# Kernel tuning notes

Hardware: AMD Instinct MI355X
Metric: run time of the kernel (lower is better)

The kernel has to match this reference:

```python
import jax, jax.numpy as jnp
import numpy as np

DIM = 1024; NH = 16; HD = DIM // NH          # head_dim = 64
E = 8; K = 2; TEMP = 1.0; HID = 1024         # routed experts / top-k / moe_inter_dim
SHID = HID * 1                               # shared expert hidden (n_shared_experts=1)
EPS = 1e-6


def _rms(x, w):
    return x * jax.lax.rsqrt(jnp.mean(x * x, axis=-1, keepdims=True) + EPS) * w


def setup_inputs() -> dict:
    key = jax.random.key(0)
    ks = jax.random.split(key, 16)
    B, S = 2, 2048
    x = jax.random.normal(ks[0], (B, S, DIM), jnp.float32)
    # RoPE table: (S, HD//2, 2) with [..., 0]=cos, [..., 1]=sin  (theta=10000)
    inv = 1.0 / (10000.0 ** (jnp.arange(0, HD, 2, dtype=jnp.float32) / HD))
    ang = jnp.arange(S, dtype=jnp.float32)[:, None] * inv[None, :]
    freqs = jnp.stack([jnp.cos(ang), jnp.sin(ang)], axis=-1)
    sc = 0.02
    W = lambda k, shape: jax.random.normal(k, shape, jnp.float32) * sc
    return dict(
        x=x, freqs=freqs,
        att_norm_w=jnp.ones((DIM,), jnp.float32),
        wq=W(ks[1], (DIM, DIM)), wk=W(ks[2], (DIM, DIM)),
        wv=W(ks[3], (DIM, DIM)), wo=W(ks[4], (DIM, DIM)),
        ffn_norm_w=jnp.ones((DIM,), jnp.float32),
        gate_w=W(ks[5], (E, DIM)),
        ew1=W(ks[6], (E, DIM, HID)), ew2=W(ks[7], (E, HID, DIM)), ew3=W(ks[8], (E, DIM, HID)),
        sw1=W(ks[9], (DIM, SHID)), sw2=W(ks[10], (SHID, DIM)), sw3=W(ks[11], (DIM, SHID)),
    )


def reference(x, freqs, att_norm_w, wq, wk, wv, wo, ffn_norm_w, gate_w,
              ew1, ew2, ew3, sw1, sw2, sw3):
    B, S, _ = x.shape
    # --- attention sub-block ---
    xn = _rms(x, att_norm_w)
    q = (xn @ wq).reshape(B, S, NH, HD)
    k = (xn @ wk).reshape(B, S, NH, HD)
    v = (xn @ wv).reshape(B, S, NH, HD)
    cos = freqs[:S, :, 0][None, :, None, :]  # (1,S,1,HD//2)
    sin = freqs[:S, :, 1][None, :, None, :]
    def rope(t):  # complex multiply on interleaved (real, imag) pairs
        t = t.reshape(B, S, NH, HD // 2, 2)
        r = t[..., 0] * cos - t[..., 1] * sin
        i = t[..., 0] * sin + t[..., 1] * cos
        return jnp.stack([r, i], axis=-1).reshape(B, S, NH, HD)
    q = rope(q); k = rope(k)
    q = q.transpose(0, 2, 1, 3); k = k.transpose(0, 2, 1, 3); v = v.transpose(0, 2, 1, 3)
    scores = jnp.einsum('bhqd,bhkd->bhqk', q, k) / np.sqrt(HD).astype(np.float32)
    probs = jax.nn.softmax(scores.astype(jnp.float32), axis=-1).astype(q.dtype)
    att = jnp.einsum('bhqk,bhkd->bhqd', probs, v).transpose(0, 2, 1, 3).reshape(B, S, DIM)
    h = x + att @ wo
    # --- MoE sub-block ---
    hn = _rms(h, ffn_norm_w).reshape(-1, DIM)  # (N, DIM), N = B*S
    N = hn.shape[0]
    gate_scores = (hn @ gate_w.T) / TEMP
    gate_probs = jax.nn.softmax(gate_scores, axis=-1)
    topk_vals, topk_idx = jax.lax.top_k(gate_probs, K)
    # expert_mask[n, e] = routing weight (0 if not in top-k)
    expert_mask = jnp.zeros((N, E), hn.dtype).at[jnp.arange(N)[:, None], topk_idx].set(topk_vals)
    # dense grouped-GEMM form of the per-expert gather/compute/scatter loop;
    # tokens not routed to expert e get weight 0 => identical math
    h1 = jnp.einsum('nd,edh->enh', hn, ew1)
    h3 = jnp.einsum('nd,edh->enh', hn, ew3)
    eo = jnp.einsum('enh,ehd->end', jax.nn.silu(h1) * h3, ew2)
    y = jnp.einsum('end,ne->nd', eo, expert_mask)
    shared = (jax.nn.silu(hn @ sw1) * (hn @ sw3)) @ sw2
    return h + (y + shared).reshape(B, S, DIM)
```

## Files before the change

kernel.cpp:

```cpp
#include <hip/hip_runtime.h>

#define DIMD 1024
#define NHEAD 16
#define HDIM 64
#define SEQ 2048
#define NBATCH 2
#define NTOK 4096
#define NEXP 8
#define HIDD 1024
#define NSLOT 8192
#define MAXTILES 72
#define FA_BQ 128
#define FA_BK 64

typedef unsigned short ushort_t;
typedef __bf16 bf16x8 __attribute__((ext_vector_type(8)));
typedef float f32x4 __attribute__((ext_vector_type(4)));
typedef unsigned short ushort8v __attribute__((ext_vector_type(8)));
typedef unsigned short ushort4v __attribute__((ext_vector_type(4)));

#define GLL16(gp, lp) __builtin_amdgcn_global_load_lds( \
    (const __attribute__((address_space(1))) unsigned int*)(gp), \
    (__attribute__((address_space(3))) unsigned int*)(lp), 16, 0, 0)

__device__ inline float bf2f(ushort_t b) {
    union { unsigned int u; float f; } v; v.u = ((unsigned int)b) << 16; return v.f;
}
__device__ inline ushort_t f2bf(float f) {
    union { float f; unsigned int u; } v; v.f = f;
    unsigned int u = v.u;
    return (ushort_t)((u + 0x7FFFu + ((u >> 16) & 1u)) >> 16);
}
__device__ inline ushort_t cvt_bf16(float f) { return f2bf(f); }
__device__ inline ushort_t cvt_bf16(ushort_t u) { return u; }

template <typename Tin>
__global__ __launch_bounds__(256) void transpose_bf16(
    const Tin* __restrict__ in, ushort_t* __restrict__ out,
    int R, int C, int ld_in, int ld_out, int nb1,
    long si1, long si2, long so1, long so2)
{
    __shared__ ushort_t tile[32][33];
    int z = blockIdx.z, z1 = z % nb1, z2 = z / nb1;
    in  += (size_t)z1 * si1 + (size_t)z2 * si2;
    out += (size_t)z1 * so1 + (size_t)z2 * so2;
    int c0 = blockIdx.x * 32, r0 = blockIdx.y * 32;
    int tx = threadIdx.x & 31, ty = threadIdx.x >> 5;
#pragma unroll
    for (int i = 0; i < 4; i++) {
        int r = r0 + ty + i * 8, c = c0 + tx;
        ushort_t v = 0;
        if (r < R && c < C) v = cvt_bf16(in[(size_t)r * ld_in + c]);
        tile[ty + i * 8][tx] = v;
    }
    __syncthreads();
#pragma unroll
    for (int i = 0; i < 4; i++) {
        int cc = c0 + ty + i * 8, rr = r0 + tx;
        if (cc < C && rr < R) out[(size_t)cc * ld_out + rr] = tile[tx][ty + i * 8];
    }
}

__global__ __launch_bounds__(256) void transpose7(
    const float* __restrict__ p0, const float* __restrict__ p1, const float* __restrict__ p2,
    const float* __restrict__ p3, const float* __restrict__ p4, const float* __restrict__ p5,
    const float* __restrict__ p6, ushort_t* __restrict__ out)
{
    __shared__ ushort_t tile[32][33];
    const float* srcs[7] = {p0, p1, p2, p3, p4, p5, p6};
    const float* in = srcs[blockIdx.z];
    ushort_t* o = out + (size_t)blockIdx.z * DIMD * DIMD;
    int c0 = blockIdx.x * 32, r0 = blockIdx.y * 32;
    int tx = threadIdx.x & 31, ty = threadIdx.x >> 5;
#pragma unroll
    for (int i = 0; i < 4; i++)
        tile[ty + i * 8][tx] = f2bf(in[(size_t)(r0 + ty + i * 8) * DIMD + c0 + tx]);
    __syncthreads();
#pragma unroll
    for (int i = 0; i < 4; i++)
        o[(size_t)(c0 + ty + i * 8) * DIMD + r0 + tx] = tile[tx][ty + i * 8];
}

__global__ __launch_bounds__(256) void rmsnorm_kernel(
    const float* __restrict__ x, const float* __restrict__ w, ushort_t* __restrict__ out)
{
    size_t row = blockIdx.x;
    const float* xr = x + row * DIMD;
    int t = threadIdx.x;
    float4 xv = ((const float4*)xr)[t];
    float ss = xv.x * xv.x + xv.y * xv.y + xv.z * xv.z + xv.w * xv.w;
    for (int o = 32; o; o >>= 1) ss += __shfl_xor(ss, o, 64);
    __shared__ float red[4];
    if ((t & 63) == 0) red[t >> 6] = ss;
    __syncthreads();
    ss = red[0] + red[1] + red[2] + red[3];
    float rs = 1.0f / sqrtf(ss / (float)DIMD + 1e-6f);
    float4 wv = ((const float4*)w)[t];
    ushort4v o;
    o[0] = f2bf(xv.x * rs * wv.x); o[1] = f2bf(xv.y * rs * wv.y);
    o[2] = f2bf(xv.z * rs * wv.z); o[3] = f2bf(xv.w * rs * wv.w);
    *(ushort4v*)(out + row * DIMD + t * 4) = o;
}

template <bool OUT_BF16, bool RESID>
__global__ __launch_bounds__(256, 2) void gemm_bt(
    const ushort_t* __restrict__ A, const ushort_t* __restrict__ B,
    void* __restrict__ Cv, const float* __restrict__ Rres,
    int M, int N, int K, int lda, int ldb, int ldc,
    int nb1, long sA1, long sA2, long sB1, long sB2, long sC1, long sC2,
    float alpha)
{
    __shared__ ushort_t lsA[128][32];
    __shared__ ushort_t lsB[128][32];
    int z = blockIdx.z, z1 = z % nb1, z2 = z / nb1;
    A += (size_t)z1 * sA1 + (size_t)z2 * sA2;
    B += (size_t)z1 * sB1 + (size_t)z2 * sB2;
    size_t coff = (size_t)z1 * sC1 + (size_t)z2 * sC2;
    int tn0 = blockIdx.x * 128, tm0 = blockIdx.y * 128;
    int t = threadIdx.x;
    int wave = t >> 6, lane = t & 63;
    int wm = (wave >> 1) * 64, wn = (wave & 1) * 64;
    int lrow = lane & 15, quad = lane >> 4;
    char* lsAb = (char*)&lsA[0][0];
    char* lsBb = (char*)&lsB[0][0];
    f32x4 acc[4][4] = {};

    for (int kt = 0; kt < K; kt += 32) {
        __syncthreads();
#pragma unroll
        for (int cc = 0; cc < 2; cc++) {
            int c = t + cc * 256;
            int r = c >> 2, kc = (c & 3) * 8;
            int ar = tm0 + r; ar = (ar < M) ? ar : (M - 1);
            GLL16(A + (size_t)ar * lda + kt + kc, lsAb + (size_t)c * 16);
            int br = tn0 + r; br = (br < N) ? br : (N - 1);
            GLL16(B + (size_t)br * ldb + kt + kc, lsBb + (size_t)c * 16);
        }
        __syncthreads();
        bf16x8 afr[4], bfr[4];
#pragma unroll
        for (int i = 0; i < 4; i++) {
            afr[i] = *(const bf16x8*)(&lsA[wm + i * 16 + lrow][quad * 8]);
            bfr[i] = *(const bf16x8*)(&lsB[wn + i * 16 + lrow][quad * 8]);
        }
#pragma unroll
        for (int mi = 0; mi < 4; mi++)
#pragma unroll
            for (int ni = 0; ni < 4; ni++)
                acc[mi][ni] = __builtin_amdgcn_mfma_f32_16x16x32_bf16(
                    afr[mi], bfr[ni], acc[mi][ni], 0, 0, 0);
    }
#pragma unroll
    for (int mi = 0; mi < 4; mi++)
#pragma unroll
        for (int ni = 0; ni < 4; ni++) {
            int col = tn0 + wn + ni * 16 + lrow;
            if (col >= N) continue;
            int row0 = tm0 + wm + mi * 16 + quad * 4;
#pragma unroll
            for (int r = 0; r < 4; r++) {
                int row = row0 + r;
                if (row >= M) continue;
                size_t idx = coff + (size_t)row * ldc + col;
                float v = acc[mi][ni][r] * alpha;
                if (RESID) v += Rres[idx];
                if (OUT_BF16) ((ushort_t*)Cv)[idx] = f2bf(v);
                else          ((float*)Cv)[idx] = v;
            }
        }
}

__global__ __launch_bounds__(256, 2) void gemm_grouped(
    const ushort_t* __restrict__ A, const ushort_t* __restrict__ Bt,
    ushort_t* __restrict__ C, const int* __restrict__ perm,
    const int* __restrict__ tile_e, const int* __restrict__ tile_r0,
    const int* __restrict__ tile_r1, const int* __restrict__ ntiles, long sBe)
{
    int tt = blockIdx.y;
    if (tt >= *ntiles) return;
    int e = tile_e[tt], r0 = tile_r0[tt], r1 = tile_r1[tt];
    const ushort_t* B = Bt + (size_t)e * sBe;
    int tn0 = blockIdx.x * 128;
    __shared__ ushort_t lsA[128][32];
    __shared__ ushort_t lsB[128][32];
    int t = threadIdx.x;
    int wave = t >> 6, lane = t & 63;
    int wm = (wave >> 1) * 64, wn = (wave & 1) * 64;
    int lrow = lane & 15, quad = lane >> 4;
    char* lsAb = (char*)&lsA[0][0];
    char* lsBb = (char*)&lsB[0][0];
    f32x4 acc[4][4] = {};

    for (int kt = 0; kt < DIMD; kt += 32) {
        __syncthreads();
#pragma unroll
        for (int cc = 0; cc < 2; cc++) {
            int c = t + cc * 256;
            int r = c >> 2, kc = (c & 3) * 8;
            int sl = r0 + r; if (sl >= r1) sl = r1 - 1;
            int ar = perm ? perm[sl] : sl;
            GLL16(A + (size_t)ar * DIMD + kt + kc, lsAb + (size_t)c * 16);
            int br = tn0 + r;
            GLL16(B + (size_t)br * DIMD + kt + kc, lsBb + (size_t)c * 16);
        }
        __syncthreads();
        bf16x8 afr[4], bfr[4];
#pragma unroll
        for (int i = 0; i < 4; i++) {
            afr[i] = *(const bf16x8*)(&lsA[wm + i * 16 + lrow][quad * 8]);
            bfr[i] = *(const bf16x8*)(&lsB[wn + i * 16 + lrow][quad * 8]);
        }
#pragma unroll
        for (int mi = 0; mi < 4; mi++)
#pragma unroll
            for (int ni = 0; ni < 4; ni++)
                acc[mi][ni] = __builtin_amdgcn_mfma_f32_16x16x32_bf16(
                    afr[mi], bfr[ni], acc[mi][ni], 0, 0, 0);
    }
#pragma unroll
    for (int mi = 0; mi < 4; mi++)
#pragma unroll
        for (int ni = 0; ni < 4; ni++) {
            int col = tn0 + wn + ni * 16 + lrow;
            int l0 = wm + mi * 16 + quad * 4;
#pragma unroll
            for (int r = 0; r < 4; r++) {
                int slot = r0 + l0 + r;
                if (slot >= r1) continue;
                C[(size_t)slot * DIMD + col] = f2bf(acc[mi][ni][r]);
            }
        }
}

__global__ __launch_bounds__(256, 2) void moe_mlp1(
    const ushort_t* __restrict__ A, const ushort_t* __restrict__ B1t, const ushort_t* __restrict__ B3t,
    ushort_t* __restrict__ C, const int* __restrict__ perm,
    const int* __restrict__ tile_e, const int* __restrict__ tile_r0,
    const int* __restrict__ tile_r1, const int* __restrict__ ntiles, long sBe)
{
    int tt = blockIdx.y;
    if (tt >= *ntiles) return;
    int e = tile_e[tt], r0 = tile_r0[tt], r1 = tile_r1[tt];
    const ushort_t* B1 = B1t + (size_t)e * sBe;
    const ushort_t* B3 = B3t + (size_t)e * sBe;
    int tn0 = blockIdx.x * 128;
    __shared__ ushort_t lsA[128][32];
    __shared__ ushort_t lsB1[128][32];
    __shared__ ushort_t lsB3[128][32];
    int t = threadIdx.x;
    int wave = t >> 6, lane = t & 63;
    int wm = (wave >> 1) * 64, wn = (wave & 1) * 64;
    int lrow = lane & 15, quad = lane >> 4;
    char* lsAb  = (char*)&lsA[0][0];
    char* lsB1b = (char*)&lsB1[0][0];
    char* lsB3b = (char*)&lsB3[0][0];
    f32x4 acc1[4][4] = {};
    f32x4 acc3[4][4] = {};

    for (int kt = 0; kt < DIMD; kt += 32) {
        __syncthreads();
#pragma unroll
        for (int cc = 0; cc < 2; cc++) {
            int c = t + cc * 256;
            int r = c >> 2, kc = (c & 3) * 8;
            int sl = r0 + r; if (sl >= r1) sl = r1 - 1;
            int ar = perm ? perm[sl] : sl;
            GLL16(A + (size_t)ar * DIMD + kt + kc, lsAb + (size_t)c * 16);
            int br = tn0 + r;
            GLL16(B1 + (size_t)br * DIMD + kt + kc, lsB1b + (size_t)c * 16);
            GLL16(B3 + (size_t)br * DIMD + kt + kc, lsB3b + (size_t)c * 16);
        }
        __syncthreads();
        bf16x8 afr[4], b1fr[4], b3fr[4];
#pragma unroll
        for (int i = 0; i < 4; i++) {
            afr[i]  = *(const bf16x8*)(&lsA[wm + i * 16 + lrow][quad * 8]);
            b1fr[i] = *(const bf16x8*)(&lsB1[wn + i * 16 + lrow][quad * 8]);
            b3fr[i] = *(const bf16x8*)(&lsB3[wn + i * 16 + lrow][quad * 8]);
        }
#pragma unroll
        for (int mi = 0; mi < 4; mi++)
#pragma unroll
            for (int ni = 0; ni < 4; ni++) {
                acc1[mi][ni] = __builtin_amdgcn_mfma_f32_16x16x32_bf16(
                    afr[mi], b1fr[ni], acc1[mi][ni], 0, 0, 0);
                acc3[mi][ni] = __builtin_amdgcn_mfma_f32_16x16x32_bf16(
                    afr[mi], b3fr[ni], acc3[mi][ni], 0, 0, 0);
            }
    }
#pragma unroll
    for (int mi = 0; mi < 4; mi++)
#pragma unroll
        for (int ni = 0; ni < 4; ni++) {
            int col = tn0 + wn + ni * 16 + lrow;
            int l0 = wm + mi * 16 + quad * 4;
#pragma unroll
            for (int r = 0; r < 4; r++) {
                int slot = r0 + l0 + r;
                if (slot >= r1) continue;
                float h1 = acc1[mi][ni][r], h3 = acc3[mi][ni][r];
                float s = h1 / (1.f + __expf(-h1));
                C[(size_t)slot * DIMD + col] = f2bf(s * h3);
            }
        }
}

__global__ __launch_bounds__(256) void rope_kernel(
    const ushort_t* __restrict__ qkv, const float* __restrict__ freqs,
    ushort_t* __restrict__ qout, ushort_t* __restrict__ kout)
{
    int s = blockIdx.x, b = blockIdx.y, t = threadIdx.x;
#pragma unroll
    for (int pp = 0; pp < 2; pp++) {
        int p = t + pp * 256;
        int hh = p >> 5, i = p & 31;
        float cs = freqs[(s * 32 + i) * 2 + 0];
        float sn = freqs[(s * 32 + i) * 2 + 1];
        size_t row = (size_t)(b * SEQ + s) * 3072;
        size_t qi = row + hh * HDIM + 2 * i;
        size_t ki = row + 1024 + hh * HDIM + 2 * i;
        size_t out_idx = ((size_t)((b * NHEAD + hh) * SEQ + s)) * HDIM + 2 * i;
        float t0 = bf2f(qkv[qi]), t1 = bf2f(qkv[qi + 1]);
        qout[out_idx]     = f2bf(t0 * cs - t1 * sn);
        qout[out_idx + 1] = f2bf(t0 * sn + t1 * cs);
        t0 = bf2f(qkv[ki]); t1 = bf2f(qkv[ki + 1]);
        kout[out_idx]     = f2bf(t0 * cs - t1 * sn);
        kout[out_idx + 1] = f2bf(t0 * sn + t1 * cs);
    }
}

__global__ __launch_bounds__(256, 4) void flash_attn(
    const ushort_t* __restrict__ q_r, const ushort_t* __restrict__ k_r,
    const ushort_t* __restrict__ vT, ushort_t* __restrict__ att)
{
    __shared__ ushort_t Kt[FA_BK][72];
    __shared__ ushort_t Vt[HDIM][72];
    __shared__ ushort_t Pt[FA_BQ][72];
    int qt = blockIdx.x, bh = blockIdx.y;
    int t = threadIdx.x, wave = t >> 6, lane = t & 63;
    int lrow = lane & 15, quad = lane >> 4;
    int qrow0 = qt * FA_BQ + wave * 32;
    const float S2 = 0.18033688f;
    const float M2 = 1.44269504f;

    const ushort_t* Qb = q_r + (size_t)bh * SEQ * HDIM;
    const ushort_t* Kb = k_r + (size_t)bh * SEQ * HDIM;
    const ushort_t* Vb = vT + (size_t)bh * HDIM * SEQ;

    bf16x8 qf[2][2];
#pragma unroll
    for (int mi = 0; mi < 2; mi++)
#pragma unroll
        for (int kk = 0; kk < 2; kk++)
            qf[mi][kk] = *(const bf16x8*)(Qb + (size_t)(qrow0 + mi * 16 + lrow) * HDIM + kk * 32 + quad * 8);

    f32x4 Oacc[2][4] = {};
    float mst[2][4], lst[2][4];
#pragma unroll
    for (int mi = 0; mi < 2; mi++)
#pragma unroll
        for (int r = 0; r < 4; r++) { mst[mi][r] = -3e38f; lst[mi][r] = 0.f; }

    for (int kc = 0; kc < SEQ / FA_BK; kc++) {
        __syncthreads();
#pragma unroll
        for (int p = 0; p < 2; p++) {
            int c = t + p * 256;
            int r = c >> 3, j = c & 7;
            *(ushort8v*)(&Kt[r][j * 8]) =
                *(const ushort8v*)(Kb + (size_t)(kc * FA_BK + r) * HDIM + j * 8);
        }
#pragma unroll
        for (int p = 0; p < 2; p++) {
            int c = t + p * 256;
            int r = c >> 3, j = c & 7;
            *(ushort8v*)(&Vt[r][j * 8]) =
                *(const ushort8v*)(Vb + (size_t)r * SEQ + kc * FA_BK + j * 8);
        }
        __syncthreads();
        f32x4 s[2][4] = {};
#pragma unroll
        for (int nj = 0; nj < 4; nj++) {
            bf16x8 bf0 = *(const bf16x8*)(&Kt[nj * 16 + lrow][quad * 8]);
            bf16x8 bf1 = *(const bf16x8*)(&Kt[nj * 16 + lrow][32 + quad * 8]);
#pragma unroll
            for (int mi = 0; mi < 2; mi++) {
                s[mi][nj] = __builtin_amdgcn_mfma_f32_16x16x32_bf16(qf[mi][0], bf0, s[mi][nj], 0, 0, 0);
                s[mi][nj] = __builtin_amdgcn_mfma_f32_16x16x32_bf16(qf[mi][1], bf1, s[mi][nj], 0, 0, 0);
            }
        }
#pragma unroll
        for (int mi = 0; mi < 2; mi++)
#pragma unroll
            for (int r = 0; r < 4; r++) {
                float rowmax = fmaxf(fmaxf(s[mi][0][r], s[mi][1][r]), fmaxf(s[mi][2][r], s[mi][3][r]));
                rowmax *= 0.125f;
#pragma unroll
                for (int o = 1; o < 16; o <<= 1) rowmax = fmaxf(rowmax, __shfl_xor(rowmax, o, 64));
                float mnew = fmaxf(mst[mi][r], rowmax);
                float alpha = __builtin_amdgcn_exp2f(M2 * (mst[mi][r] - mnew));
                float mb = M2 * mnew;
                float rsum = 0.f;
#pragma unroll
                for (int nj = 0; nj < 4; nj++) {
                    float pv = __builtin_amdgcn_exp2f(s[mi][nj][r] * S2 - mb);
                    s[mi][nj][r] = pv;
                    rsum += pv;
                }
#pragma unroll
                for (int o = 1; o < 16; o <<= 1) rsum += __shfl_xor(rsum, o, 64);
                lst[mi][r] = lst[mi][r] * alpha + rsum;
                mst[mi][r] = mnew;
#pragma unroll
                for (int nj = 0; nj < 4; nj++) Oacc[mi][nj][r] *= alpha;
            }
#pragma unroll
        for (int mi = 0; mi < 2; mi++)
#pragma unroll
            for (int nj = 0; nj < 4; nj++)
#pragma unroll
                for (int r = 0; r < 4; r++)
                    Pt[wave * 32 + mi * 16 + quad * 4 + r][nj * 16 + lrow] = f2bf(s[mi][nj][r]);
#pragma unroll
        for (int kk = 0; kk < 2; kk++) {
            bf16x8 af0 = *(const bf16x8*)(&Pt[wave * 32 + lrow][kk * 32 + quad * 8]);
            bf16x8 af1 = *(const bf16x8*)(&Pt[wave * 32 + 16 + lrow][kk * 32 + quad * 8]);
#pragma unroll
            for (int nj = 0; nj < 4; nj++) {
                bf16x8 bf = *(const bf16x8*)(&Vt[nj * 16 + lrow][kk * 32 + quad * 8]);
                Oacc[0][nj] = __builtin_amdgcn_mfma_f32_16x16x32_bf16(af0, bf, Oacc[0][nj], 0, 0, 0);
                Oacc[1][nj] = __builtin_amdgcn_mfma_f32_16x16x32_bf16(af1, bf, Oacc[1][nj], 0, 0, 0);
            }
        }
    }
    int b = bh >> 4, h = bh & 15;
#pragma unroll
    for (int mi = 0; mi < 2; mi++)
#pragma unroll
        for (int r = 0; r < 4; r++) {
            int srow = qrow0 + mi * 16 + quad * 4 + r;
            float inv = 1.0f / lst[mi][r];
#pragma unroll
            for (int nj = 0; nj < 4; nj++) {
                int d = nj * 16 + lrow;
                att[((size_t)(b * SEQ + srow)) * DIMD + h * HDIM + d] = f2bf(Oacc[mi][nj][r] * inv);
            }
        }
}

__global__ __launch_bounds__(256) void gate_kernel(
    const float* __restrict__ h, const float* __restrict__ gw, const float* __restrict__ fw,
    int* __restrict__ tok_e, float* __restrict__ tok_w)
{
    int tok = blockIdx.x, t = threadIdx.x;
    const float* hr = h + (size_t)tok * DIMD;
    float ssq = 0.f;
    for (int k = t; k < DIMD; k += 256) { float v = hr[k]; ssq += v * v; }
    for (int o = 32; o; o >>= 1) ssq += __shfl_xor(ssq, o, 64);
    __shared__ float red[4];
    if ((t & 63) == 0) red[t >> 6] = ssq;
    __syncthreads();
    ssq = red[0] + red[1] + red[2] + red[3];
    float rs = 1.0f / sqrtf(ssq / (float)DIMD + 1e-6f);
    int e = t >> 5, lane = t & 31;
    float sc = 0.f;
    for (int k = lane; k < DIMD; k += 32) sc += hr[k] * rs * fw[k] * gw[e * DIMD + k];
    for (int o = 16; o; o >>= 1) sc += __shfl_down(sc, o, 32);
    __shared__ float se[NEXP];
    if (lane == 0) se[e] = sc;
    __syncthreads();
    if (t == 0) {
        float mx = se[0];
        for (int i = 1; i < NEXP; i++) mx = fmaxf(mx, se[i]);
        float pr[NEXP], sum = 0.f;
        for (int i = 0; i < NEXP; i++) { pr[i] = __expf(se[i] - mx); sum += pr[i]; }
        float inv = 1.0f / sum;
        for (int i = 0; i < NEXP; i++) pr[i] *= inv;
        int i0 = 0;
        for (int i = 1; i < NEXP; i++) if (pr[i] > pr[i0]) i0 = i;
        int i1 = -1;
        for (int i = 0; i < NEXP; i++) { if (i == i0) continue; if (i1 < 0 || pr[i] > pr[i1]) i1 = i; }
        tok_e[tok * 2] = i0; tok_e[tok * 2 + 1] = i1;
        tok_w[tok * 2] = pr[i0]; tok_w[tok * 2 + 1] = pr[i1];
    }
}

__global__ __launch_bounds__(1024) void route_kernel(
    const int* __restrict__ tok_e, int* __restrict__ ntiles,
    int* __restrict__ tile_e, int* __restrict__ tile_r0, int* __restrict__ tile_r1,
    int* __restrict__ perm, int* __restrict__ slot_of)
{
    __shared__ int hist[NEXP][1024];
    __shared__ int totals[NEXP], offs[NEXP];
    int t = threadIdx.x;
    int e_loc[8];
    int c[NEXP];
#pragma unroll
    for (int e = 0; e < NEXP; e++) c[e] = 0;
#pragma unroll
    for (int j = 0; j < 8; j++) { int e = tok_e[t * 8 + j]; e_loc[j] = e; c[e]++; }
#pragma unroll
    for (int e = 0; e < NEXP; e++) hist[e][t] = c[e];
    __syncthreads();
    int wv = t >> 6, ln = t & 63;
    if (wv < NEXP) {
        int run = 0;
        for (int ch = 0; ch < 16; ch++) {
            int v = hist[wv][ch * 64 + ln];
            int x = v;
#pragma unroll
            for (int o = 1; o < 64; o <<= 1) { int y = __shfl_up(x, o, 64); if (ln >= o) x += y; }
            hist[wv][ch * 64 + ln] = run + x - v;
            run += __shfl(x, 63, 64);
        }
        if (ln == 0) totals[wv] = run;
    }
    __syncthreads();
    if (t == 0) {
        int off = 0, nt = 0;
        for (int e = 0; e < NEXP; e++) {
            offs[e] = off;
            int cc = totals[e];
            for (int r = 0; r < cc; r += 128) {
                tile_e[nt] = e;
                tile_r0[nt] = off + r;
                tile_r1[nt] = off + ((r + 128 < cc) ? (r + 128) : cc);
                nt++;
            }
            off += cc;
        }
        *ntiles = nt;
    }
    __syncthreads();
    int c2[NEXP];
#pragma unroll
    for (int e = 0; e < NEXP; e++) c2[e] = 0;
#pragma unroll
    for (int j = 0; j < 8; j++) {
        int e = e_loc[j];
        int slot = offs[e] + hist[e][t] + c2[e]++;
        perm[slot] = (t * 8 + j) >> 1;
        slot_of[t * 8 + j] = slot;
    }
}

__global__ __launch_bounds__(256) void silu_pair(
    const ushort_t* __restrict__ s13, ushort_t* __restrict__ o)
{
    int i = blockIdx.x * 256 + threadIdx.x;
    int stride = gridDim.x * 256;
    for (; i < NTOK * DIMD; i += stride) {
        int r = i >> 10, c = i & 1023;
        float a = bf2f(s13[(size_t)r * 2048 + c]);
        float b = bf2f(s13[(size_t)r * 2048 + 1024 + c]);
        o[i] = f2bf(a / (1.f + __expf(-a)) * b);
    }
}

__global__ __launch_bounds__(256) void combine_kernel(
    const float* __restrict__ shf, const ushort_t* __restrict__ eo,
    const int* __restrict__ slot_of, const float* __restrict__ tok_w, float* __restrict__ out)
{
    int tok = blockIdx.x, t = threadIdx.x;
    int s0 = slot_of[tok * 2], s1 = slot_of[tok * 2 + 1];
    float w0 = tok_w[tok * 2], w1 = tok_w[tok * 2 + 1];
    const ushort_t* e0 = eo + (size_t)s0 * DIMD;
    const ushort_t* e1 = eo + (size_t)s1 * DIMD;
    size_t base = (size_t)tok * DIMD;
    for (int k = t; k < DIMD; k += 256)
        out[base + k] = shf[base + k] + w0 * bf2f(e0[k]) + w1 * bf2f(e1[k]);
}

__global__ void report_ws(float* out, float v) { out[0] = v; }

extern "C" void kernel_launch(void* const* d_in, const int* in_sizes, int n_in,
                              void* d_out, int out_size, void* d_ws, size_t ws_size,
                              hipStream_t stream)
{
    const float* x     = (const float*)d_in[0];
    const float* freqs = (const float*)d_in[1];
    const float* attw  = (const float*)d_in[2];
    const float* wq    = (const float*)d_in[3];
    const float* wk    = (const float*)d_in[4];
    const float* wv    = (const float*)d_in[5];
    const float* wo    = (const float*)d_in[6];
    const float* ffnw  = (const float*)d_in[7];
    const float* gatew = (const float*)d_in[8];
    const float* ew1   = (const float*)d_in[9];
    const float* ew2   = (const float*)d_in[10];
    const float* ew3   = (const float*)d_in[11];
    const float* sw1   = (const float*)d_in[12];
    const float* sw2   = (const float*)d_in[13];
    const float* sw3   = (const float*)d_in[14];
    float* out = (float*)d_out;

    char* ws = (char*)d_ws;
    const size_t MB = 1024 * 1024;
    const size_t MM = (size_t)DIMD * DIMD;
    if (ws_size < 160 * MB) { report_ws<<<1, 1, 0, stream>>>(out, (float)ws_size); return; }

    ushort_t* wqT  = (ushort_t*)(ws + 0 * MB);
    ushort_t* woT  = (ushort_t*)(ws + 6 * MB);
    ushort_t* sw1T = (ushort_t*)(ws + 8 * MB);
    ushort_t* sw2T = (ushort_t*)(ws + 12 * MB);
    ushort_t* ew1T = (ushort_t*)(ws + 14 * MB);
    ushort_t* ew2T = (ushort_t*)(ws + 30 * MB);
    ushort_t* ew3T = (ushort_t*)(ws + 46 * MB);
    float*    hbuf = (float*)   (ws + 62 * MB);
    ushort_t* hn   = (ushort_t*)(ws + 78 * MB);
    ushort_t* actb = (ushort_t*)(ws + 86 * MB);
    ushort_t* eo   = (ushort_t*)(ws + 102 * MB);
    ushort_t* xn   = (ushort_t*)(ws + 86 * MB);
    ushort_t* qkv  = (ushort_t*)(ws + 94 * MB);
    ushort_t* q_r  = (ushort_t*)(ws + 118 * MB);
    ushort_t* k_r  = (ushort_t*)(ws + 126 * MB);
    ushort_t* vTb  = (ushort_t*)(ws + 134 * MB);
    ushort_t* att  = (ushort_t*)(ws + 142 * MB);
    ushort_t* s13  = (ushort_t*)(ws + 118 * MB);
    ushort_t* shb  = (ushort_t*)(ws + 134 * MB);
    float*    shf  = (float*)   (ws + 142 * MB);
    int*      meta = (int*)     (ws + 158 * MB);

    int* ntiles  = meta;
    int* tile_e  = meta + 32;     int* tile_r0 = meta + 104;  int* tile_r1 = meta + 176;
    int* tok_e   = meta + 256;    int* slot_of = meta + 256 + 8192;
    int* permv   = meta + 256 + 16384;
    float* tok_w = (float*)(meta + 256 + 24576);

    transpose7<<<dim3(32, 32, 7), 256, 0, stream>>>(wq, wk, wv, wo, sw1, sw3, sw2, wqT);
    transpose_bf16<float><<<dim3(32, 32, 8), 256, 0, stream>>>(ew1, ew1T, DIMD, DIMD, DIMD, DIMD, 8, (long)MM, 0, (long)MM, 0);
    transpose_bf16<float><<<dim3(32, 32, 8), 256, 0, stream>>>(ew2, ew2T, DIMD, DIMD, DIMD, DIMD, 8, (long)MM, 0, (long)MM, 0);
    transpose_bf16<float><<<dim3(32, 32, 8), 256, 0, stream>>>(ew3, ew3T, DIMD, DIMD, DIMD, DIMD, 8, (long)MM, 0, (long)MM, 0);

    rmsnorm_kernel<<<NTOK, 256, 0, stream>>>(x, attw, xn);
    gemm_bt<true, false><<<dim3(24, 32, 1), 256, 0, stream>>>(xn, wqT, qkv, nullptr,
        NTOK, 3072, DIMD, DIMD, DIMD, 3072, 1, 0, 0, 0, 0, 0, 0, 1.0f);
    rope_kernel<<<dim3(SEQ, NBATCH), 256, 0, stream>>>(qkv, freqs, q_r, k_r);
    transpose_bf16<ushort_t><<<dim3(HDIM / 32, SEQ / 32, NBATCH * NHEAD), 256, 0, stream>>>(
        qkv + 2048, vTb, SEQ, HDIM, 3072, SEQ, NHEAD,
        (long)HDIM, (long)SEQ * 3072, (long)HDIM * SEQ, (long)NHEAD * HDIM * SEQ);

    flash_attn<<<dim3(SEQ / FA_BQ, NBATCH * NHEAD), 256, 0, stream>>>(q_r, k_r, vTb, att);

    gemm_bt<false, true><<<dim3(8, 32, 1), 256, 0, stream>>>(att, woT, hbuf, x,
        NTOK, DIMD, DIMD, DIMD, DIMD, DIMD, 1, 0, 0, 0, 0, 0, 0, 1.0f);
    rmsnorm_kernel<<<NTOK, 256, 0, stream>>>(hbuf, ffnw, hn);

    gate_kernel<<<NTOK, 256, 0, stream>>>(hbuf, gatew, ffnw, tok_e, tok_w);
    route_kernel<<<1, 1024, 0, stream>>>(tok_e, ntiles, tile_e, tile_r0, tile_r1, permv, slot_of);

    moe_mlp1<<<dim3(8, MAXTILES), 256, 0, stream>>>(hn, ew1T, ew3T, actb, permv,
        tile_e, tile_r0, tile_r1, ntiles, (long)MM);
    gemm_grouped<<<dim3(8, MAXTILES), 256, 0, stream>>>(actb, ew2T, eo, nullptr,
        tile_e, tile_r0, tile_r1, ntiles, (long)MM);

    gemm_bt<true, false><<<dim3(16, 32, 1), 256, 0, stream>>>(hn, sw1T, s13, nullptr,
        NTOK, 2048, DIMD, DIMD, DIMD, 2048, 1, 0, 0, 0, 0, 0, 0, 1.0f);
    silu_pair<<<2048, 256, 0, stream>>>(s13, shb);
    gemm_bt<false, true><<<dim3(8, 32, 1), 256, 0, stream>>>(shb, sw2T, shf, hbuf,
        NTOK, DIMD, DIMD, DIMD, DIMD, DIMD, 1, 0, 0, 0, 0, 0, 0, 1.0f);

    combine_kernel<<<NTOK, 256, 0, stream>>>(shf, eo, slot_of, tok_w, out);
}
```

Measured before the change: 708.9 us.

## Retile flash attention to 64 query rows and 128-key chunks per block

Reshapes the flash attention tiling so each block handles 64 query rows, with one 16-row MFMA tile per wave, while streaming 128 keys per iteration instead of 64. Each iteration now runs 8 score tiles and 4 PV k-steps, with V and P LDS tiles widened to match. The goal is to halve the number of online-softmax rescale and barrier steps over the sequence and to launch twice as many blocks. In exchange, each K and V fragment read from LDS is reused across only one query tile instead of two, the total K/V global traffic doubles, and the occupancy hint drops to 3 blocks per CU.

```diff
diff --git a/kernel.cpp b/kernel.cpp
--- a/kernel.cpp
+++ b/kernel.cpp
@@ -10,8 +10,8 @@
 #define HIDD 1024
 #define NSLOT 8192
 #define MAXTILES 72
-#define FA_BQ 128
-#define FA_BK 64
+#define FA_BQ 64
+#define FA_BK 128
 
 typedef unsigned short ushort_t;
 typedef __bf16 bf16x8 __attribute__((ext_vector_type(8)));
@@ -329,17 +329,17 @@
     }
 }
 
-__global__ __launch_bounds__(256, 4) void flash_attn(
+__global__ __launch_bounds__(256, 3) void flash_attn(
     const ushort_t* __restrict__ q_r, const ushort_t* __restrict__ k_r,
     const ushort_t* __restrict__ vT, ushort_t* __restrict__ att)
 {
     __shared__ ushort_t Kt[FA_BK][72];
-    __shared__ ushort_t Vt[HDIM][72];
-    __shared__ ushort_t Pt[FA_BQ][72];
+    __shared__ ushort_t Vt[HDIM][136];
+    __shared__ ushort_t Pt[FA_BQ][136];
     int qt = blockIdx.x, bh = blockIdx.y;
     int t = threadIdx.x, wave = t >> 6, lane = t & 63;
     int lrow = lane & 15, quad = lane >> 4;
-    int qrow0 = qt * FA_BQ + wave * 32;
+    int qrow0 = qt * FA_BQ + wave * 16;
     const float S2 = 0.18033688f;
     const float M2 = 1.44269504f;
 
@@ -347,105 +347,92 @@
     const ushort_t* Kb = k_r + (size_t)bh * SEQ * HDIM;
     const ushort_t* Vb = vT + (size_t)bh * HDIM * SEQ;
 
-    bf16x8 qf[2][2];
-#pragma unroll
-    for (int mi = 0; mi < 2; mi++)
-#pragma unroll
-        for (int kk = 0; kk < 2; kk++)
-            qf[mi][kk] = *(const bf16x8*)(Qb + (size_t)(qrow0 + mi * 16 + lrow) * HDIM + kk * 32 + quad * 8);
-
-    f32x4 Oacc[2][4] = {};
-    float mst[2][4], lst[2][4];
-#pragma unroll
-    for (int mi = 0; mi < 2; mi++)
-#pragma unroll
-        for (int r = 0; r < 4; r++) { mst[mi][r] = -3e38f; lst[mi][r] = 0.f; }
+    bf16x8 qf[2];
+#pragma unroll
+    for (int kk = 0; kk < 2; kk++)
+        qf[kk] = *(const bf16x8*)(Qb + (size_t)(qrow0 + lrow) * HDIM + kk * 32 + quad * 8);
+
+    f32x4 Oacc[4] = {};
+    float mst[4], lst[4];
+#pragma unroll
+    for (int r = 0; r < 4; r++) { mst[r] = -3e38f; lst[r] = 0.f; }
 
     for (int kc = 0; kc < SEQ / FA_BK; kc++) {
         __syncthreads();
 #pragma unroll
-        for (int p = 0; p < 2; p++) {
+        for (int p = 0; p < 4; p++) {
             int c = t + p * 256;
             int r = c >> 3, j = c & 7;
             *(ushort8v*)(&Kt[r][j * 8]) =
                 *(const ushort8v*)(Kb + (size_t)(kc * FA_BK + r) * HDIM + j * 8);
         }
 #pragma unroll
-        for (int p = 0; p < 2; p++) {
+        for (int p = 0; p < 4; p++) {
             int c = t + p * 256;
-            int r = c >> 3, j = c & 7;
+            int r = c >> 4, j = c & 15;
             *(ushort8v*)(&Vt[r][j * 8]) =
                 *(const ushort8v*)(Vb + (size_t)r * SEQ + kc * FA_BK + j * 8);
         }
         __syncthreads();
-        f32x4 s[2][4] = {};
-#pragma unroll
-        for (int nj = 0; nj < 4; nj++) {
+        f32x4 s[8] = {};
+#pragma unroll
+        for (int nj = 0; nj < 8; nj++) {
             bf16x8 bf0 = *(const bf16x8*)(&Kt[nj * 16 + lrow][quad * 8]);
             bf16x8 bf1 = *(const bf16x8*)(&Kt[nj * 16 + lrow][32 + quad * 8]);
-#pragma unroll
-            for (int mi = 0; mi < 2; mi++) {
-                s[mi][nj] = __builtin_amdgcn_mfma_f32_16x16x32_bf16(qf[mi][0], bf0, s[mi][nj], 0, 0, 0);
-                s[mi][nj] = __builtin_amdgcn_mfma_f32_16x16x32_bf16(qf[mi][1], bf1, s[mi][nj], 0, 0, 0);
+            s[nj] = __builtin_amdgcn_mfma_f32_16x16x32_bf16(qf[0], bf0, s[nj], 0, 0, 0);
+            s[nj] = __builtin_amdgcn_mfma_f32_16x16x32_bf16(qf[1], bf1, s[nj], 0, 0, 0);
+        }
+#pragma unroll
+        for (int r = 0; r < 4; r++) {
+            float rowmax = -3e38f;
+#pragma unroll
+            for (int nj = 0; nj < 8; nj++) rowmax = fmaxf(rowmax, s[nj][r]);
+            rowmax *= 0.125f;
+#pragma unroll
+            for (int o = 1; o < 16; o <<= 1) rowmax = fmaxf(rowmax, __shfl_xor(rowmax, o, 64));
+            float mnew = fmaxf(mst[r], rowmax);
+            float alpha = __builtin_amdgcn_exp2f(M2 * (mst[r] - mnew));
+            float mb = M2 * mnew;
+            float rsum = 0.f;
+#pragma unroll
+            for (int nj = 0; nj < 8; nj++) {
+                float pv = __builtin_amdgcn_exp2f(s[nj][r] * S2 - mb);
+                s[nj][r] = pv;
+                rsum += pv;
             }
-        }
-#pragma unroll
-        for (int mi = 0; mi < 2; mi++)
-#pragma unroll
-            for (int r = 0; r < 4; r++) {
-                float rowmax = fmaxf(fmaxf(s[mi][0][r], s[mi][1][r]), fmaxf(s[mi][2][r], s[mi][3][r]));
-                rowmax *= 0.125f;
-#pragma unroll
-                for (int o = 1; o < 16; o <<= 1) rowmax = fmaxf(rowmax, __shfl_xor(rowmax, o, 64));
-                float mnew = fmaxf(mst[mi][r], rowmax);
-                float alpha = __builtin_amdgcn_exp2f(M2 * (mst[mi][r] - mnew));
-                float mb = M2 * mnew;
-                float rsum = 0.f;
-#pragma unroll
-                for (int nj = 0; nj < 4; nj++) {
-                    float pv = __builtin_amdgcn_exp2f(s[mi][nj][r] * S2 - mb);
-                    s[mi][nj][r] = pv;
-                    rsum += pv;
-                }
-#pragma unroll
-                for (int o = 1; o < 16; o <<= 1) rsum += __shfl_xor(rsum, o, 64);
-                lst[mi][r] = lst[mi][r] * alpha + rsum;
-                mst[mi][r] = mnew;
-#pragma unroll
-                for (int nj = 0; nj < 4; nj++) Oacc[mi][nj][r] *= alpha;
-            }
-#pragma unroll
-        for (int mi = 0; mi < 2; mi++)
-#pragma unroll
-            for (int nj = 0; nj < 4; nj++)
-#pragma unroll
-                for (int r = 0; r < 4; r++)
-                    Pt[wave * 32 + mi * 16 + quad * 4 + r][nj * 16 + lrow] = f2bf(s[mi][nj][r]);
-#pragma unroll
-        for (int kk = 0; kk < 2; kk++) {
-            bf16x8 af0 = *(const bf16x8*)(&Pt[wave * 32 + lrow][kk * 32 + quad * 8]);
-            bf16x8 af1 = *(const bf16x8*)(&Pt[wave * 32 + 16 + lrow][kk * 32 + quad * 8]);
+#pragma unroll
+            for (int o = 1; o < 16; o <<= 1) rsum += __shfl_xor(rsum, o, 64);
+            lst[r] = lst[r] * alpha + rsum;
+            mst[r] = mnew;
+#pragma unroll
+            for (int nj = 0; nj < 4; nj++) Oacc[nj][r] *= alpha;
+        }
+#pragma unroll
+        for (int nj = 0; nj < 8; nj++)
+#pragma unroll
+            for (int r = 0; r < 4; r++)
+                Pt[wave * 16 + quad * 4 + r][nj * 16 + lrow] = f2bf(s[nj][r]);
+#pragma unroll
+        for (int kk = 0; kk < 4; kk++) {
+            bf16x8 af = *(const bf16x8*)(&Pt[wave * 16 + lrow][kk * 32 + quad * 8]);
 #pragma unroll
             for (int nj = 0; nj < 4; nj++) {
                 bf16x8 bf = *(const bf16x8*)(&Vt[nj * 16 + lrow][kk * 32 + quad * 8]);
-                Oacc[0][nj] = __builtin_amdgcn_mfma_f32_16x16x32_bf16(af0, bf, Oacc[0][nj], 0, 0, 0);
-                Oacc[1][nj] = __builtin_amdgcn_mfma_f32_16x16x32_bf16(af1, bf, Oacc[1][nj], 0, 0, 0);
+                Oacc[nj] = __builtin_amdgcn_mfma_f32_16x16x32_bf16(af, bf, Oacc[nj], 0, 0, 0);
             }
         }
     }
     int b = bh >> 4, h = bh & 15;
 #pragma unroll
-    for (int mi = 0; mi < 2; mi++)
-#pragma unroll
-        for (int r = 0; r < 4; r++) {
-            int srow = qrow0 + mi * 16 + quad * 4 + r;
-            float inv = 1.0f / lst[mi][r];
-#pragma unroll
-            for (int nj = 0; nj < 4; nj++) {
-                int d = nj * 16 + lrow;
-                att[((size_t)(b * SEQ + srow)) * DIMD + h * HDIM + d] = f2bf(Oacc[mi][nj][r] * inv);
-            }
-        }
+    for (int r = 0; r < 4; r++) {
+        int srow = qrow0 + quad * 4 + r;
+        float inv = 1.0f / lst[r];
+#pragma unroll
+        for (int nj = 0; nj < 4; nj++) {
+            int d = nj * 16 + lrow;
+            att[((size_t)(b * SEQ + srow)) * DIMD + h * HDIM + d] = f2bf(Oacc[nj][r] * inv);
+        }
+    }
 }
 
 __global__ __launch_bounds__(256) void gate_kernel(
```

Result: faster. 646.8 us (-8.8%).
